# Optimization experiments

Hardware: AMD Instinct MI355X
Metric: run time of the kernel (lower is better)

## Reference

```python
import jax, jax.numpy as jnp
import numpy as np

B, S, D, H, DH = 2, 4096, 768, 12, 64
BS, NB, L, FF, VOCAB = 16, 256, 2, 3072, 50358
SCALE = 1.0 / np.sqrt(DH)


def _ln(x, g, b, eps=1e-12):
    m = jnp.mean(x, -1, keepdims=True)
    v = jnp.var(x, -1, keepdims=True)
    return (x - m) * jax.lax.rsqrt(v + eps) * g + b


def _make_key_block_idx(seed=0):
    rng = np.random.default_rng(seed)
    idx = np.zeros((NB, 7), np.int32)
    allb = np.arange(NB)
    for i in range(NB):
        req = sorted({0, NB - 1, max(i - 1, 0), i, min(i + 1, NB - 1)})
        pool = np.setdiff1d(allb, req)
        extra = rng.choice(pool, size=7 - len(req), replace=False)
        idx[i] = np.concatenate([req, extra])
    return jnp.asarray(idx)


def _sparse_attn(q, k, v, key_idx):
    # q,k,v: [B,H,NB,BS,DH]; key_idx: [NB,7]
    kg = k[:, :, key_idx].reshape(B, H, NB, 7 * BS, DH)  # gather key blocks
    vg = v[:, :, key_idx].reshape(B, H, NB, 7 * BS, DH)
    s = jnp.einsum('bhnqd,bhnkd->bhnqk', q, kg) * SCALE
    o = jnp.einsum('bhnqk,bhnkd->bhnqd', jax.nn.softmax(s, -1), vg)
    # first/last query blocks: full (global) attention over all keys
    qe = q[:, :, jnp.array([0, NB - 1])]                 # [B,H,2,BS,DH]
    kf = k.reshape(B, H, S, DH)
    vf = v.reshape(B, H, S, DH)
    se = jnp.einsum('bhgqd,bhkd->bhgqk', qe, kf) * SCALE
    oe = jnp.einsum('bhgqk,bhkd->bhgqd', jax.nn.softmax(se, -1), vf)
    o = o.at[:, :, 0].set(oe[:, :, 0]).at[:, :, NB - 1].set(oe[:, :, 1])
    # [B,H,NB,BS,DH] -> [B,S,D]
    return o.transpose(0, 2, 3, 1, 4).reshape(B, S, D)


def setup_inputs():
    key = jax.random.key(0)
    ks = iter(jax.random.split(key, 24))
    n = lambda sh, s=0.02: jax.random.normal(next(ks), sh, jnp.float32) * s
    inp = {
        'input_ids': jax.random.randint(next(ks), (B, S), 0, VOCAB),
        'key_block_idx': _make_key_block_idx(),
        'embed': n((VOCAB, D)),
        'Wqkv': n((L, D, 3 * D)), 'bqkv': jnp.zeros((L, 3 * D)),
        'Wo': n((L, D, D)), 'bo': jnp.zeros((L, D)),
        'ln1_g': jnp.ones((L, D)), 'ln1_b': jnp.zeros((L, D)),
        'Wff1': n((L, D, FF)), 'bff1': jnp.zeros((L, FF)),
        'Wff2': n((L, FF, D)), 'bff2': jnp.zeros((L, D)),
        'ln2_g': jnp.ones((L, D)), 'ln2_b': jnp.zeros((L, D)),
        'Wp': n((D, D)), 'bp': jnp.zeros((D,)),
        'start_w': jax.random.normal(next(ks), (D,)),
        'end_w': jax.random.normal(next(ks), (D,)),
        'd1_W': n((D, 20)), 'd1_b': jnp.zeros((20,)),
        'd2_W': n((20, 2)), 'd2_b': jnp.zeros((2,)),
    }
    return inp


def reference(input_ids, key_block_idx, embed, Wqkv, bqkv, Wo, bo, ln1_g, ln1_b,
              Wff1, bff1, Wff2, bff2, ln2_g, ln2_b, Wp, bp, start_w, end_w,
              d1_W, d1_b, d2_W, d2_b):
    x = embed[input_ids]                                  # [B,S,D]
    for l in range(L):
        qkv = x @ Wqkv[l] + bqkv[l]
        q, k, v = jnp.split(qkv, 3, axis=-1)
        blk = lambda t: t.reshape(B, NB, BS, H, DH).transpose(0, 3, 1, 2, 4)
        a = _sparse_attn(blk(q), blk(k), blk(v), key_block_idx)
        x = _ln(x + a @ Wo[l] + bo[l], ln1_g[l], ln1_b[l])
        h = jax.nn.gelu(x @ Wff1[l] + bff1[l]) @ Wff2[l] + bff2[l]
        x = _ln(x + h, ln2_g[l], ln2_b[l])
    pool = jnp.tanh(x[:, 0] @ Wp + bp)                    # BigBird pooler
    start_probs = jax.nn.softmax(x @ start_w, -1)         # [B,S]
    end_probs = jax.nn.softmax(x @ end_w, -1)
    d = (pool[0] @ d1_W + d1_b) @ d2_W + d2_b             # no ReLU, as in source
    disc = jax.nn.softmax(d, -1)
    return start_probs, end_probs, disc
```

## Files before the change

### kernel.cpp

```cpp
#include <hip/hip_runtime.h>
#include <hip/hip_bf16.h>
#include <math.h>

#define B_   2
#define S_   4096
#define D_   768
#define H_   12
#define DH_  64
#define BS_  16
#define NB_  256
#define FF_  3072
#define BT_  (B_ * S_)
#define SCALE_F 0.125f

#define NSPLIT 32
#define TILES_PER_SPLIT (NB_ / NSPLIT)
#define NEDGE (B_ * H_ * 2)
#define NSPARSE (B_ * H_ * NB_)

#define DKS 8
#define DKC (D_ / DKS)

typedef _Float16 f16x8 __attribute__((ext_vector_type(8)));
typedef _Float16 f16x4 __attribute__((ext_vector_type(4)));
typedef _Float16 f16x2 __attribute__((ext_vector_type(2)));
typedef float    f32x4 __attribute__((ext_vector_type(4)));

#define SV2(v, k) __builtin_shufflevector(v, v, k, (k) + 1)

__device__ __forceinline__ float dot2acc(f16x2 a, f16x2 b, float c)
{
#if __has_builtin(__builtin_amdgcn_fdot2)
    return __builtin_amdgcn_fdot2(a, b, c, false);
#else
    return c + (float)a[0] * (float)b[0] + (float)a[1] * (float)b[1];
#endif
}

#define GLD16(gp, lp) __builtin_amdgcn_global_load_lds( \
    (const __attribute__((address_space(1))) void*)(gp), \
    (__attribute__((address_space(3))) void*)(lp), 16, 0, 0)

__device__ __forceinline__ float fast_tanh(float z)
{
    float az = fabsf(z);
    float t = __expf(-2.0f * az);
    float r = (1.0f - t) / (1.0f + t);
    return z < 0.f ? -r : r;
}

__device__ __forceinline__ float gelu_tanh(float v)
{
    float v3 = v * v * v;
    return 0.5f * v * (1.0f + fast_tanh(0.79788456080286535588f * (v + 0.044715f * v3)));
}

struct WSeg { const float* src; _Float16* dst; int K; int N; int start; };
struct WSegs { WSeg s[8]; int total; };

__global__ __launch_bounds__(256) void prep_all(
    WSegs segs, const int* __restrict__ ids, const float* __restrict__ emb,
    _Float16* __restrict__ xh)
{
    int bt = blockIdx.x;
    int t = threadIdx.x;
    if (bt < segs.total) {
        __shared__ float tile[32][33];
        int si = 0;
#pragma unroll
        for (int u = 1; u < 8; ++u)
            if (bt >= segs.s[u].start) si = u;
        const WSeg& sg = segs.s[si];
        int tid = bt - sg.start;
        int tn = sg.N >> 5;
        int n0 = (tid % tn) * 32;
        int k0 = (tid / tn) * 32;

        int r = t >> 5, c = t & 31;
#pragma unroll
        for (int rr = 0; rr < 32; rr += 8)
            tile[r + rr][c] = sg.src[(size_t)(k0 + r + rr) * sg.N + n0 + c];
        __syncthreads();
#pragma unroll
        for (int rr = 0; rr < 32; rr += 8)
            sg.dst[(size_t)(n0 + r + rr) * sg.K + k0 + c] = (_Float16)tile[c][r + rr];
    } else {
        int row = bt - segs.total;
        int id = ids[row];
        const float* src = emb + (size_t)id * D_;
        _Float16* dst16 = xh + (size_t)row * D_;
        for (int d = t; d < D_; d += 256)
            dst16[d] = (_Float16)src[d];
    }
}

template<int ACT, int OUT16>
__global__ __launch_bounds__(256) void gemm_f16(
    const _Float16* __restrict__ A, const _Float16* __restrict__ Wt,
    const float* __restrict__ bias, void* __restrict__ Cp,
    int M, int N, int K)
{
    __shared__ __attribute__((aligned(16))) _Float16 As[128 * 64];
    __shared__ __attribute__((aligned(16))) _Float16 Bs[128 * 64];

    int t = threadIdx.x;
    int w = t >> 6, l = t & 63;
    int bm = blockIdx.y * 128, bn = blockIdx.x * 128;
    int wr = (w >> 1) * 64, wc = (w & 1) * 64;

    f32x4 acc[4][4];
#pragma unroll
    for (int i = 0; i < 4; ++i)
#pragma unroll
        for (int j = 0; j < 4; ++j) acc[i][j] = (f32x4){0.f, 0.f, 0.f, 0.f};

    const _Float16* gA[4];
    const _Float16* gB[4];
#pragma unroll
    for (int q = 0; q < 4; ++q) {
        int m = w * 4 + q;
        int row = m * 8 + (l >> 3);
        int sc = (l & 7) ^ (row & 7);
        gA[q] = A  + (size_t)(bm + row) * K + sc * 8;
        gB[q] = Wt + (size_t)(bn + row) * K + sc * 8;
    }

    int aoff[2][4], boff[2][4];
#pragma unroll
    for (int kk = 0; kk < 2; ++kk)
#pragma unroll
        for (int i = 0; i < 4; ++i) {
            int ar = wr + i * 16 + (l & 15);
            int ch = (kk * 4 + (l >> 4)) ^ (l & 7);
            aoff[kk][i] = ar * 64 + ch * 8;
            int br = wc + i * 16 + (l & 15);
            boff[kk][i] = br * 64 + ch * 8;
        }

    for (int k0 = 0; k0 < K; k0 += 64) {
#pragma unroll
        for (int q = 0; q < 4; ++q) {
            int m = w * 4 + q;
            GLD16(gA[q] + k0, As + m * 512);
            GLD16(gB[q] + k0, Bs + m * 512);
        }
        __syncthreads();

        f16x8 af[2][4], bf[2][4];
#pragma unroll
        for (int kk = 0; kk < 2; ++kk)
#pragma unroll
            for (int i = 0; i < 4; ++i) {
                af[kk][i] = *(const f16x8*)(As + aoff[kk][i]);
                bf[kk][i] = *(const f16x8*)(Bs + boff[kk][i]);
            }
#pragma unroll
        for (int kk = 0; kk < 2; ++kk)
#pragma unroll
            for (int i = 0; i < 4; ++i)
#pragma unroll
                for (int j = 0; j < 4; ++j)
                    acc[i][j] = __builtin_amdgcn_mfma_f32_16x16x32_f16(
                        af[kk][i], bf[kk][j], acc[i][j], 0, 0, 0);
        __syncthreads();
    }

#pragma unroll
    for (int i = 0; i < 4; ++i) {
        int rowb = bm + wr + i * 16 + ((l >> 4) << 2);
#pragma unroll
        for (int j = 0; j < 4; ++j) {
            int col = bn + wc + j * 16 + (l & 15);
            float bv = bias[col];
#pragma unroll
            for (int r = 0; r < 4; ++r) {
                float v = acc[i][j][r] + bv;
                if (ACT) v = gelu_tanh(v);
                if (OUT16)
                    ((_Float16*)Cp)[(size_t)(rowb + r) * N + col] = (_Float16)v;
                else
                    ((float*)Cp)[(size_t)(rowb + r) * N + col] = v;
            }
        }
    }
}

template<int NT, bool EDGE>
__device__ __forceinline__ void attn_block(
    const _Float16* __restrict__ qkv, const int* __restrict__ key_idx,
    _Float16* __restrict__ outp, float* __restrict__ pm,
    float* __restrict__ pl, float* __restrict__ pacc,
    int b, int h, int n, int split, int be,
    _Float16 (*qs)[72], _Float16 (*ks)[16][72],
    _Float16 (*vpl)[8][64][2], _Float16 (*ps16)[24])
{
    int t = threadIdx.x;
    int i = t >> 4;
    int c = t & 15;
    int c4 = c * 4;

    *(f16x4*)&qs[i][c4] =
        *(const f16x4*)&qkv[((size_t)(b * S_ + n * BS_ + i)) * (3 * D_) + h * DH_ + c4];
    int kb0 = EDGE ? split * NT : key_idx[n * 7];
    const _Float16* kp0 = qkv + ((size_t)(b * S_ + kb0 * BS_ + i)) * (3 * D_) + D_ + h * DH_;
    f16x4 kr = *(const f16x4*)(kp0 + c4);
    f16x4 vr = *(const f16x4*)(kp0 + D_ + c4);
    __syncthreads();

    f16x8 qv[8];
#pragma unroll
    for (int d0 = 0; d0 < 8; ++d0) qv[d0] = *(const f16x8*)&qs[i][d0 * 8];

    *(f16x4*)&ks[0][i][c4] = kr;
#pragma unroll
    for (int u = 0; u < 4; ++u) vpl[0][i >> 1][c4 + u][i & 1] = vr[u];
    if (NT > 1) {
        int kb1 = EDGE ? (split * NT + 1) : key_idx[n * 7 + 1];
        const _Float16* kp1 = qkv + ((size_t)(b * S_ + kb1 * BS_ + i)) * (3 * D_) + D_ + h * DH_;
        kr = *(const f16x4*)(kp1 + c4);
        vr = *(const f16x4*)(kp1 + D_ + c4);
    }
    __syncthreads();

    float m_old = -1e30f, lsum = 0.f;
    float acc0 = 0.f, acc1 = 0.f, acc2 = 0.f, acc3 = 0.f;
    const f16x2 one2 = {(_Float16)1.f, (_Float16)1.f};

#pragma unroll 1
    for (int jj = 0; jj < NT; ++jj) {
        int cur = jj & 1;
        if (jj + 1 < NT) {
            *(f16x4*)&ks[cur ^ 1][i][c4] = kr;
#pragma unroll
            for (int u = 0; u < 4; ++u) vpl[cur ^ 1][i >> 1][c4 + u][i & 1] = vr[u];
        }
        if (jj + 2 < NT) {
            int kb2 = EDGE ? (split * NT + jj + 2) : key_idx[n * 7 + jj + 2];
            const _Float16* kp2 = qkv + ((size_t)(b * S_ + kb2 * BS_ + i)) * (3 * D_) + D_ + h * DH_;
            kr = *(const f16x4*)(kp2 + c4);
            vr = *(const f16x4*)(kp2 + D_ + c4);
        }

        __builtin_amdgcn_s_setprio(1);
        float s0 = 0.f, s1 = 0.f;
#pragma unroll
        for (int d0 = 0; d0 < 8; ++d0) {
            f16x8 kv = *(const f16x8*)&ks[cur][c][d0 * 8];
            s0 = dot2acc(SV2(qv[d0], 0), SV2(kv, 0), s0);
            s1 = dot2acc(SV2(qv[d0], 2), SV2(kv, 2), s1);
            s0 = dot2acc(SV2(qv[d0], 4), SV2(kv, 4), s0);
            s1 = dot2acc(SV2(qv[d0], 6), SV2(kv, 6), s1);
        }
        float s = (s0 + s1) * SCALE_F;

        float rm = s;
#pragma unroll
        for (int off = 8; off; off >>= 1) rm = fmaxf(rm, __shfl_xor(rm, off, 64));
        float m_new = fmaxf(m_old, rm);
        float p = __expf(s - m_new);

        ps16[i][c] = (_Float16)p;
        f16x8 plo = *(const f16x8*)&ps16[i][0];
        f16x8 phi = *(const f16x8*)&ps16[i][8];

        float rs = 0.f;
        rs = dot2acc(SV2(plo, 0), one2, rs);
        rs = dot2acc(SV2(plo, 2), one2, rs);
        rs = dot2acc(SV2(plo, 4), one2, rs);
        rs = dot2acc(SV2(plo, 6), one2, rs);
        rs = dot2acc(SV2(phi, 0), one2, rs);
        rs = dot2acc(SV2(phi, 2), one2, rs);
        rs = dot2acc(SV2(phi, 4), one2, rs);
        rs = dot2acc(SV2(phi, 6), one2, rs);

        float corr = __expf(m_old - m_new);
        lsum = lsum * corr + rs;
        acc0 *= corr; acc1 *= corr; acc2 *= corr; acc3 *= corr;

#define PVJ(JP, PSRC, OFF)                                            \
        {                                                             \
            f16x8 vv = *(const f16x8*)&vpl[cur][JP][c4][0];           \
            f16x2 pp = SV2(PSRC, OFF);                                \
            acc0 = dot2acc(pp, SV2(vv, 0), acc0);                     \
            acc1 = dot2acc(pp, SV2(vv, 2), acc1);                     \
            acc2 = dot2acc(pp, SV2(vv, 4), acc2);                     \
            acc3 = dot2acc(pp, SV2(vv, 6), acc3);                     \
        }
        PVJ(0, plo, 0) PVJ(1, plo, 2) PVJ(2, plo, 4) PVJ(3, plo, 6)
        PVJ(4, phi, 0) PVJ(5, phi, 2) PVJ(6, phi, 4) PVJ(7, phi, 6)
#undef PVJ
        __builtin_amdgcn_s_setprio(0);
        m_old = m_new;
        __syncthreads();
    }

    if (EDGE) {
        int psx = (be * NSPLIT + split) * 16 + i;
        if (c == 0) { pm[psx] = m_old; pl[psx] = lsum; }
        float* pd = pacc + (size_t)psx * 64 + c4;
        pd[0] = acc0; pd[1] = acc1; pd[2] = acc2; pd[3] = acc3;
    } else {
        float inv = 1.f / lsum;
        _Float16* dst = outp + ((size_t)(b * S_ + n * BS_ + i)) * D_ + h * DH_ + c4;
        dst[0] = (_Float16)(acc0 * inv);
        dst[1] = (_Float16)(acc1 * inv);
        dst[2] = (_Float16)(acc2 * inv);
        dst[3] = (_Float16)(acc3 * inv);
    }
}

__global__ __launch_bounds__(256) void attn_fused(
    const _Float16* __restrict__ qkv, const int* __restrict__ key_idx,
    _Float16* __restrict__ outp, float* __restrict__ pm,
    float* __restrict__ pl, float* __restrict__ pacc)
{
    __shared__ __attribute__((aligned(16))) _Float16 qs[16][72];
    __shared__ __attribute__((aligned(16))) _Float16 ks[2][16][72];
    __shared__ __attribute__((aligned(16))) _Float16 vpl[2][8][64][2];
    __shared__ __attribute__((aligned(16))) _Float16 ps16[16][24];

    int bi = blockIdx.x;
    if (bi < NSPARSE) {
        int n = bi % NB_;
        if (n == 0 || n == NB_ - 1) return;
        int h = (bi / NB_) % H_;
        int b = bi / (NB_ * H_);
        attn_block<7, false>(qkv, key_idx, outp, nullptr, nullptr, nullptr,
                             b, h, n, 0, 0, qs, ks, vpl, ps16);
    } else {
        int ei = bi - NSPARSE;
        int split = ei % NSPLIT;
        int be = ei / NSPLIT;
        int e = be & 1;
        int h = (be >> 1) % H_;
        int b = be / (2 * H_);
        int n = e ? (NB_ - 1) : 0;
        attn_block<TILES_PER_SPLIT, true>(qkv, nullptr, nullptr, pm, pl, pacc,
                                          b, h, n, split, be, qs, ks, vpl, ps16);
    }
}

__global__ __launch_bounds__(256) void attn_edge_combine(
    const float* __restrict__ pm, const float* __restrict__ pl,
    const float* __restrict__ pacc, _Float16* __restrict__ outp)
{
    int be = blockIdx.x;
    int e = be & 1;
    int h = (be >> 1) % H_;
    int b = be / (2 * H_);
    int n = e ? (NB_ - 1) : 0;

    int t = threadIdx.x;
    int i = t >> 4;
    int c = t & 15;

    float M = -1e30f;
#pragma unroll 4
    for (int s = 0; s < NSPLIT; ++s)
        M = fmaxf(M, pm[(be * NSPLIT + s) * 16 + i]);

    float L = 0.f;
    float acc[4] = {0.f, 0.f, 0.f, 0.f};
    for (int s = 0; s < NSPLIT; ++s) {
        int ps = (be * NSPLIT + s) * 16 + i;
        float wgt = __expf(pm[ps] - M);
        L += pl[ps] * wgt;
#pragma unroll
        for (int u = 0; u < 4; ++u) acc[u] += pacc[(size_t)ps * 64 + c * 4 + u] * wgt;
    }

    float inv = 1.f / L;
    _Float16* dst = outp + ((size_t)(b * S_ + n * BS_ + i)) * D_ + h * DH_ + c * 4;
#pragma unroll
    for (int u = 0; u < 4; ++u) dst[u] = (_Float16)(acc[u] * inv);
}

template<int WRITE32>
__global__ __launch_bounds__(256) void add_ln_kernel(
    _Float16* __restrict__ xh, const _Float16* __restrict__ g,
    const float* __restrict__ gamma, const float* __restrict__ beta,
    float* __restrict__ x32)
{
    int row = blockIdx.x;
    int t = threadIdx.x;
    _Float16* xr = xh + (size_t)row * D_;
    const _Float16* gr = g + (size_t)row * D_;

    float v[3];
    float s = 0.f, s2 = 0.f;
#pragma unroll
    for (int r = 0; r < 3; ++r) {
        int d = t + 256 * r;
        v[r] = (float)xr[d] + (float)gr[d];
        s += v[r];
        s2 += v[r] * v[r];
    }
#pragma unroll
    for (int off = 32; off; off >>= 1) {
        s  += __shfl_xor(s, off, 64);
        s2 += __shfl_xor(s2, off, 64);
    }
    __shared__ float sA[4], sB[4];
    int wave = t >> 6, lane = t & 63;
    if (lane == 0) { sA[wave] = s; sB[wave] = s2; }
    __syncthreads();
    s  = sA[0] + sA[1] + sA[2] + sA[3];
    s2 = sB[0] + sB[1] + sB[2] + sB[3];
    float mean = s * (1.0f / D_);
    float var = s2 * (1.0f / D_) - mean * mean;
    float rstd = rsqrtf(var + 1e-12f);
#pragma unroll
    for (int r = 0; r < 3; ++r) {
        int d = t + 256 * r;
        float o = (v[r] - mean) * rstd * gamma[d] + beta[d];
        xr[d] = (_Float16)o;
        if (WRITE32) x32[(size_t)row * D_ + d] = o;
    }
}

__global__ __launch_bounds__(256) void heads_fused(
    const float* __restrict__ x, const float* __restrict__ sw,
    const float* __restrict__ ew, const float* __restrict__ Wp,
    float* __restrict__ sl, float* __restrict__ el,
    float* __restrict__ partial)
{
    int bi = blockIdx.x;
    int t = threadIdx.x;
    if (bi < 2048) {
        int wave = t >> 6, lane = t & 63;
        int row = bi * 4 + wave;
        const float* xr = x + (size_t)row * D_;
        float a = 0.f, e = 0.f;
        for (int d = lane; d < D_; d += 64) {
            float xv = xr[d];
            a += xv * sw[d];
            e += xv * ew[d];
        }
#pragma unroll
        for (int off = 32; off; off >>= 1) {
            a += __shfl_xor(a, off, 64);
            e += __shfl_xor(e, off, 64);
        }
        if (lane == 0) { sl[row] = a; el[row] = e; }
    } else {
        int ei = bi - 2048;
        int jb = ei % 3;
        int ks = ei / 3;
        int j = jb * 256 + t;
        int k0 = ks * DKC;

        __shared__ float xs[DKC];
        if (t < DKC) xs[t] = x[k0 + t];
        __syncthreads();

        float s = 0.f;
#pragma unroll 8
        for (int kk = 0; kk < DKC; ++kk)
            s += xs[kk] * Wp[(size_t)(k0 + kk) * D_ + j];
        partial[ks * D_ + j] = s;
    }
}

__global__ __launch_bounds__(256) void final_fused(
    const float* __restrict__ sl, const float* __restrict__ el,
    const float* __restrict__ partial, const float* __restrict__ bp,
    const float* __restrict__ d1W, const float* __restrict__ d1b,
    const float* __restrict__ d2W, const float* __restrict__ d2b,
    float* __restrict__ outp)
{
    int r = blockIdx.x;
    int t = threadIdx.x;
    if (r < 4) {
        const float* src = (r < 2 ? sl : el) + (size_t)(r & 1) * S_;
        float* dst = outp + (r < 2 ? 0 : BT_) + (size_t)(r & 1) * S_;
        int wave = t >> 6, lane = t & 63;
        __shared__ float sm[4], ss[4];

        float m = -1e30f;
        for (int k = t; k < S_; k += 256) m = fmaxf(m, src[k]);
#pragma unroll
        for (int off = 32; off; off >>= 1) m = fmaxf(m, __shfl_xor(m, off, 64));
        if (lane == 0) sm[wave] = m;
        __syncthreads();
        m = fmaxf(fmaxf(sm[0], sm[1]), fmaxf(sm[2], sm[3]));

        float s = 0.f;
        for (int k = t; k < S_; k += 256) s += __expf(src[k] - m);
#pragma unroll
        for (int off = 32; off; off >>= 1) s += __shfl_xor(s, off, 64);
        if (lane == 0) ss[wave] = s;
        __syncthreads();
        s = ss[0] + ss[1] + ss[2] + ss[3];

        float inv = 1.f / s;
        for (int k = t; k < S_; k += 256) dst[k] = __expf(src[k] - m) * inv;
    } else {
        __shared__ float pool[D_];
        __shared__ float h1[20];
        float* out2 = outp + 2 * BT_;
        for (int j = t; j < D_; j += 256) {
            float s = bp[j];
#pragma unroll
            for (int ks = 0; ks < DKS; ++ks) s += partial[ks * D_ + j];
            pool[j] = tanhf(s);
        }
        __syncthreads();
        if (t < 20) {
            float s = d1b[t];
            for (int k = 0; k < D_; ++k) s += pool[k] * d1W[k * 20 + t];
            h1[t] = s;
        }
        __syncthreads();
        if (t == 0) {
            float d0 = d2b[0], d1v = d2b[1];
#pragma unroll
            for (int u = 0; u < 20; ++u) {
                d0  += h1[u] * d2W[u * 2 + 0];
                d1v += h1[u] * d2W[u * 2 + 1];
            }
            float m = fmaxf(d0, d1v);
            float e0 = __expf(d0 - m), e1 = __expf(d1v - m);
            float inv = 1.f / (e0 + e1);
            out2[0] = e0 * inv;
            out2[1] = e1 * inv;
        }
    }
}

extern "C" void kernel_launch(void* const* d_in, const int* in_sizes, int n_in,
                              void* d_out, int out_size, void* d_ws, size_t ws_size,
                              hipStream_t stream)
{
    const int*   ids   = (const int*)d_in[0];
    const int*   kbi   = (const int*)d_in[1];
    const float* emb   = (const float*)d_in[2];
    const float* Wqkv  = (const float*)d_in[3];
    const float* bqkv  = (const float*)d_in[4];
    const float* Wo    = (const float*)d_in[5];
    const float* bo    = (const float*)d_in[6];
    const float* ln1g  = (const float*)d_in[7];
    const float* ln1b  = (const float*)d_in[8];
    const float* Wff1  = (const float*)d_in[9];
    const float* bff1  = (const float*)d_in[10];
    const float* Wff2  = (const float*)d_in[11];
    const float* bff2  = (const float*)d_in[12];
    const float* ln2g  = (const float*)d_in[13];
    const float* ln2b  = (const float*)d_in[14];
    const float* Wp    = (const float*)d_in[15];
    const float* bp    = (const float*)d_in[16];
    const float* sw    = (const float*)d_in[17];
    const float* ew    = (const float*)d_in[18];
    const float* d1W   = (const float*)d_in[19];
    const float* d1b   = (const float*)d_in[20];
    const float* d2W   = (const float*)d_in[21];
    const float* d2b   = (const float*)d_in[22];
    float* outp = (float*)d_out;

    float* ws   = (float*)d_ws;
    float* x    = ws;
    float* xbf  = x   + (size_t)BT_ * D_;
    float* r1f  = xbf + (size_t)BT_ * D_ / 2;
    float* abf  = r1f + (size_t)BT_ * FF_ / 2;
    float* r2   = abf + (size_t)BT_ * D_ / 2;
    float* wtf  = r2  + (size_t)BT_ * D_;
    float* sl   = wtf + 7077888;
    float* el   = sl  + BT_;
    float* dpar = el  + BT_;

    _Float16* xh    = (_Float16*)xbf;
    _Float16* qkv16 = (_Float16*)r1f;
    _Float16* h16   = (_Float16*)r1f;
    _Float16* ab    = (_Float16*)abf;
    float* pm   = r2;
    float* pl   = r2 + NEDGE * NSPLIT * 16;
    float* pacc = pl + NEDGE * NSPLIT * 16;
    _Float16* g16 = (_Float16*)r2;

    _Float16* Wt    = (_Float16*)wtf;
    _Float16* WqkvT = Wt;
    _Float16* WoT   = WqkvT + (size_t)2 * 2304 * 768;
    _Float16* Wff1T = WoT   + (size_t)2 * 768 * 768;
    _Float16* Wff2T = Wff1T + (size_t)2 * 3072 * 768;

    WSegs segs;
    int start = 0;
    for (int l = 0; l < 2; ++l) {
        int base = l * 4;
        segs.s[base + 0] = { Wqkv + (size_t)l * 768 * 2304,
                             WqkvT + (size_t)l * 2304 * 768, 768, 2304, start };
        start += (2304 / 32) * (768 / 32);
        segs.s[base + 1] = { Wo + (size_t)l * 768 * 768,
                             WoT + (size_t)l * 768 * 768, 768, 768, start };
        start += (768 / 32) * (768 / 32);
        segs.s[base + 2] = { Wff1 + (size_t)l * 768 * 3072,
                             Wff1T + (size_t)l * 3072 * 768, 768, 3072, start };
        start += (3072 / 32) * (768 / 32);
        segs.s[base + 3] = { Wff2 + (size_t)l * 3072 * 768,
                             Wff2T + (size_t)l * 768 * 3072, 3072, 768, start };
        start += (768 / 32) * (3072 / 32);
    }
    segs.total = start;

    prep_all<<<segs.total + BT_, 256, 0, stream>>>(segs, ids, emb, xh);

    for (int l = 0; l < 2; ++l) {
        gemm_f16<0,1><<<dim3(2304/128, BT_/128), 256, 0, stream>>>(
            xh, WqkvT + (size_t)l * 2304 * 768, bqkv + (size_t)l * 3 * D_,
            qkv16, BT_, 3 * D_, D_);
        attn_fused<<<NSPARSE + NEDGE * NSPLIT, 256, 0, stream>>>(
            qkv16, kbi, ab, pm, pl, pacc);
        attn_edge_combine<<<NEDGE, 256, 0, stream>>>(pm, pl, pacc, ab);
        gemm_f16<0,1><<<dim3(768/128, BT_/128), 256, 0, stream>>>(
            ab, WoT + (size_t)l * 768 * 768, bo + (size_t)l * D_,
            g16, BT_, D_, D_);
        add_ln_kernel<0><<<BT_, 256, 0, stream>>>(
            xh, g16, ln1g + (size_t)l * D_, ln1b + (size_t)l * D_, nullptr);
        gemm_f16<1,1><<<dim3(3072/128, BT_/128), 256, 0, stream>>>(
            xh, Wff1T + (size_t)l * 3072 * 768, bff1 + (size_t)l * FF_,
            h16, BT_, FF_, D_);
        gemm_f16<0,1><<<dim3(768/128, BT_/128), 256, 0, stream>>>(
            h16, Wff2T + (size_t)l * 768 * 3072, bff2 + (size_t)l * D_,
            g16, BT_, D_, FF_);
        if (l == 1)
            add_ln_kernel<1><<<BT_, 256, 0, stream>>>(
                xh, g16, ln2g + (size_t)l * D_, ln2b + (size_t)l * D_, x);
        else
            add_ln_kernel<0><<<BT_, 256, 0, stream>>>(
                xh, g16, ln2g + (size_t)l * D_, ln2b + (size_t)l * D_, nullptr);
    }

    heads_fused<<<2048 + 3 * DKS, 256, 0, stream>>>(x, sw, ew, Wp, sl, el, dpar);
    final_fused<<<5, 256, 0, stream>>>(sl, el, dpar, bp, d1W, d1b, d2W, d2b, outp);
}
```

Before: 672.9 us.

## Switch GEMM to 32x32x16 MFMA tiles and vectorize weight transpose

```diff
diff --git a/kernel.cpp b/kernel.cpp
--- a/kernel.cpp
+++ b/kernel.cpp
@@ -25,6 +25,7 @@
 typedef _Float16 f16x4 __attribute__((ext_vector_type(4)));
 typedef _Float16 f16x2 __attribute__((ext_vector_type(2)));
 typedef float    f32x4 __attribute__((ext_vector_type(4)));
+typedef float    f32x16 __attribute__((ext_vector_type(16)));
 
 #define SV2(v, k) __builtin_shufflevector(v, v, k, (k) + 1)
 
@@ -76,14 +77,24 @@
         int n0 = (tid % tn) * 32;
         int k0 = (tid / tn) * 32;
 
-        int r = t >> 5, c = t & 31;
-#pragma unroll
-        for (int rr = 0; rr < 32; rr += 8)
-            tile[r + rr][c] = sg.src[(size_t)(k0 + r + rr) * sg.N + n0 + c];
-        __syncthreads();
-#pragma unroll
-        for (int rr = 0; rr < 32; rr += 8)
-            sg.dst[(size_t)(n0 + r + rr) * sg.K + k0 + c] = (_Float16)tile[c][r + rr];
+        {
+            int r = t >> 3, c = (t & 7) * 4;
+            f32x4 v = *(const f32x4*)&sg.src[(size_t)(k0 + r) * sg.N + n0 + c];
+            tile[r][c + 0] = v[0];
+            tile[r][c + 1] = v[1];
+            tile[r][c + 2] = v[2];
+            tile[r][c + 3] = v[3];
+        }
+        __syncthreads();
+        {
+            int r = t >> 3, c = (t & 7) * 4;
+            f16x4 o;
+            o[0] = (_Float16)tile[c + 0][r];
+            o[1] = (_Float16)tile[c + 1][r];
+            o[2] = (_Float16)tile[c + 2][r];
+            o[3] = (_Float16)tile[c + 3][r];
+            *(f16x4*)&sg.dst[(size_t)(n0 + r) * sg.K + k0 + c] = o;
+        }
     } else {
         int row = bt - segs.total;
         int id = ids[row];
@@ -108,11 +119,13 @@
     int bm = blockIdx.y * 128, bn = blockIdx.x * 128;
     int wr = (w >> 1) * 64, wc = (w & 1) * 64;
 
-    f32x4 acc[4][4];
-#pragma unroll
-    for (int i = 0; i < 4; ++i)
-#pragma unroll
-        for (int j = 0; j < 4; ++j) acc[i][j] = (f32x4){0.f, 0.f, 0.f, 0.f};
+    f32x16 acc[2][2];
+#pragma unroll
+    for (int i = 0; i < 2; ++i)
+#pragma unroll
+        for (int j = 0; j < 2; ++j)
+#pragma unroll
+            for (int r = 0; r < 16; ++r) acc[i][j][r] = 0.f;
 
     const _Float16* gA[4];
     const _Float16* gB[4];
@@ -125,17 +138,16 @@
         gB[q] = Wt + (size_t)(bn + row) * K + sc * 8;
     }
 
-    int aoff[2][4], boff[2][4];
-#pragma unroll
-    for (int kk = 0; kk < 2; ++kk)
-#pragma unroll
-        for (int i = 0; i < 4; ++i) {
-            int ar = wr + i * 16 + (l & 15);
-            int ch = (kk * 4 + (l >> 4)) ^ (l & 7);
-            aoff[kk][i] = ar * 64 + ch * 8;
-            int br = wc + i * 16 + (l & 15);
-            boff[kk][i] = br * 64 + ch * 8;
-        }
+    int aoff[4][2], boff[4][2];
+#pragma unroll
+    for (int kk = 0; kk < 4; ++kk) {
+        int ch = (kk * 2 + (l >> 5)) ^ (l & 7);
+#pragma unroll
+        for (int f = 0; f < 2; ++f) {
+            aoff[kk][f] = (wr + f * 32 + (l & 31)) * 64 + ch * 8;
+            boff[kk][f] = (wc + f * 32 + (l & 31)) * 64 + ch * 8;
+        }
+    }
 
     for (int k0 = 0; k0 < K; k0 += 64) {
 #pragma unroll
@@ -146,40 +158,42 @@
         }
         __syncthreads();
 
-        f16x8 af[2][4], bf[2][4];
-#pragma unroll
-        for (int kk = 0; kk < 2; ++kk)
-#pragma unroll
-            for (int i = 0; i < 4; ++i) {
-                af[kk][i] = *(const f16x8*)(As + aoff[kk][i]);
-                bf[kk][i] = *(const f16x8*)(Bs + boff[kk][i]);
+#pragma unroll
+        for (int kk = 0; kk < 4; ++kk) {
+            f16x8 af[2], bf[2];
+#pragma unroll
+            for (int f = 0; f < 2; ++f) {
+                af[f] = *(const f16x8*)(As + aoff[kk][f]);
+                bf[f] = *(const f16x8*)(Bs + boff[kk][f]);
             }
 #pragma unroll
-        for (int kk = 0; kk < 2; ++kk)
-#pragma unroll
-            for (int i = 0; i < 4; ++i)
-#pragma unroll
-                for (int j = 0; j < 4; ++j)
-                    acc[i][j] = __builtin_amdgcn_mfma_f32_16x16x32_f16(
-                        af[kk][i], bf[kk][j], acc[i][j], 0, 0, 0);
-        __syncthreads();
-    }
-
-#pragma unroll
-    for (int i = 0; i < 4; ++i) {
-        int rowb = bm + wr + i * 16 + ((l >> 4) << 2);
-#pragma unroll
-        for (int j = 0; j < 4; ++j) {
-            int col = bn + wc + j * 16 + (l & 15);
+            for (int i = 0; i < 2; ++i)
+#pragma unroll
+                for (int j = 0; j < 2; ++j)
+                    acc[i][j] = __builtin_amdgcn_mfma_f32_32x32x16_f16(
+                        af[i], bf[j], acc[i][j], 0, 0, 0);
+        }
+        __syncthreads();
+    }
+
+#pragma unroll
+    for (int i = 0; i < 2; ++i) {
+#pragma unroll
+        for (int j = 0; j < 2; ++j) {
+            int col = bn + wc + j * 32 + (l & 31);
             float bv = bias[col];
 #pragma unroll
-            for (int r = 0; r < 4; ++r) {
-                float v = acc[i][j][r] + bv;
-                if (ACT) v = gelu_tanh(v);
-                if (OUT16)
-                    ((_Float16*)Cp)[(size_t)(rowb + r) * N + col] = (_Float16)v;
-                else
-                    ((float*)Cp)[(size_t)(rowb + r) * N + col] = v;
+            for (int rg = 0; rg < 4; ++rg) {
+                int row0 = bm + wr + i * 32 + 8 * rg + 4 * (l >> 5);
+#pragma unroll
+                for (int r = 0; r < 4; ++r) {
+                    float v = acc[i][j][rg * 4 + r] + bv;
+                    if (ACT) v = gelu_tanh(v);
+                    if (OUT16)
+                        ((_Float16*)Cp)[(size_t)(row0 + r) * N + col] = (_Float16)v;
+                    else
+                        ((float*)Cp)[(size_t)(row0 + r) * N + col] = v;
+                }
             }
         }
     }
```

New measurement: 638.4 us. 5.1% less time.
